# Performance work log

Measured on AMD Instinct MI355X. Metric: run time of the kernel, lower is better.

## Reference

```python
import jax, jax.numpy as jnp
import numpy as np

# Module config (matches init_kwargs)
G, K, S = 64, 3, 2          # base patch size, num scales, scale factor
B, H, W, C = 64, 512, 512, 3
HG, HL = 128, 128
D_IN = K * G * G * C


def setup_inputs() -> dict:
    key = jax.random.key(0)
    kx, kl, k1, k2 = jax.random.split(key, 4)
    x = jax.random.normal(kx, (B, H, W, C), dtype=jnp.float32)
    # glimpse locations in [-1, 1)
    l = jax.random.uniform(kl, (B, 2), minval=-1.0, maxval=1.0, dtype=jnp.float32)
    # fc1: phi (D_IN -> HG); fc2: l (2 -> HL). PyTorch-Linear-like scale.
    W1 = jax.random.normal(k1, (D_IN, HG), dtype=jnp.float32) / np.sqrt(D_IN)
    b1 = jnp.zeros((HG,), dtype=jnp.float32)
    W2 = jax.random.normal(k2, (2, HL), dtype=jnp.float32) / np.sqrt(2.0)
    b2 = jnp.zeros((HL,), dtype=jnp.float32)
    return {"x": x, "l": l, "W1": W1, "b1": b1, "W2": W2, "b2": b2}


def _extract_glimpse(x, l):
    """Retina: k multi-scale patches centered at l, resized to (G,G).
    Returns (B, K, G, G, C)."""
    sizes = [G * S**i for i in range(K)]              # 64, 128, 256
    pad = sizes[-1] // 2 + 1                          # pad once for largest scale
    xp = jnp.pad(x, ((0, 0), (pad, pad), (pad, pad), (0, 0)))
    # denormalize: [-1,1] -> [0,H], truncated to int (torch .long())
    coords = (0.5 * (l + 1.0) * H).astype(jnp.int32)  # (B,2): col0=x, col1=y
    patches = []
    for size in sizes:
        fy = coords[:, 1] - size // 2 + pad
        fx = coords[:, 0] - size // 2 + pad

        def slice_one(img, y0, x0, size=size):
            return jax.lax.dynamic_slice(img, (y0, x0, 0), (size, size, C))

        p = jax.vmap(slice_one)(xp, fy, fx)           # (B, size, size, C)
        f = size // G
        if f > 1:  # downsample by integer factor via average pooling
            p = p.reshape(B, G, f, G, f, C).mean(axis=(2, 4))
        patches.append(p)
    return jnp.stack(patches, axis=1)                 # (B, K, G, G, C)


def reference(x, l, W1, b1, W2, b2):
    phi = _extract_glimpse(x, l).reshape(x.shape[0], -1)   # (B, K*G*G*C)
    phi_out = jax.nn.relu(phi @ W1 + b1)                   # (B, HG)
    l_out = jax.nn.relu(l @ W2 + b2)                       # (B, HL)
    return jax.nn.relu(jnp.concatenate([phi_out, l_out], axis=1))
```

## Files before the change

kernel.cpp:

```cpp
#include <hip/hip_runtime.h>
#include <hip/hip_bf16.h>

#define G_     64
#define NK     3
#define NB     64
#define IH     512
#define IW     512
#define NC     3
#define HG_    128
#define HL_    128
#define D_IN_    (NK * G_ * G_ * NC)
#define D_SCALE  (G_ * G_ * NC)
#define KCH      128
#define NCHUNK   (D_IN_ / KCH)
#define BSPLIT   4
#define NBLK     (NCHUNK * BSPLIT)

__global__ void zero_acc(float* __restrict__ acc) {
    int i = blockIdx.x * 256 + threadIdx.x;
    if (i < NB * HG_) acc[i] = 0.0f;
}

template <int F>
__device__ __forceinline__ void scale_body(
    const float* __restrict__ x, const float* __restrict__ l,
    const float* __restrict__ W1, float* __restrict__ acc,
    int roff, int d0, int b0,
    float (&phi_s)[16][KCH], int* cx_s, int* cy_s)
{
    const int tid = threadIdx.x;
    if (tid < 16) {
        float lx = l[(b0 + tid) * 2 + 0];
        float ly = l[(b0 + tid) * 2 + 1];
        cx_s[tid] = (int)((0.5f * (lx + 1.0f)) * 512.0f);
        cy_s[tid] = (int)((0.5f * (ly + 1.0f)) * 512.0f);
    }
    __syncthreads();

    const int dd   = tid & (KCH - 1);
    const int jb0  = (tid >> 7) * 8;
    const int r    = roff + dd;
    const int gy   = r / (G_ * NC);
    const int rem  = r - gy * (G_ * NC);
    const int gx   = rem / NC;
    const int c    = rem - gx * NC;
    constexpr float inv = 1.0f / (float)(F * F);
    constexpr int JU = (F == 4) ? 2 : 8;

#pragma unroll 1
    for (int jo = 0; jo < 8; jo += JU) {
        float sums[JU];
#pragma unroll
        for (int ji = 0; ji < JU; ++ji) {
            const int jb = jb0 + jo + ji;
            const int b  = b0 + jb;
            const int by = cy_s[jb] - 32 * F + gy * F;
            const int bx = cx_s[jb] - 32 * F + gx * F;
            const float* bimg = x + (size_t)b * (IH * IW * NC) + c;
            float s = 0.0f;
#pragma unroll
            for (int dy = 0; dy < F; ++dy) {
                const int y = by + dy;
                const bool yok = (unsigned)y < (unsigned)IH;
#pragma unroll
                for (int dx = 0; dx < F; ++dx) {
                    const int xx = bx + dx;
                    const bool ok = yok && ((unsigned)xx < (unsigned)IW);
                    s += ok ? bimg[(size_t)y * (IW * NC) + xx * NC] : 0.0f;
                }
            }
            sums[ji] = s;
        }
#pragma unroll
        for (int ji = 0; ji < JU; ++ji)
            phi_s[jb0 + jo + ji][dd] = sums[ji] * inv;
    }
    __syncthreads();

    const int h0 = (tid & 31) * 4;
    const int bl = (tid >> 5) * 2;
    float a0[4] = {0, 0, 0, 0}, a1[4] = {0, 0, 0, 0};
    const float* wp = W1 + (size_t)d0 * HG_ + h0;
    const float4* prow0 = (const float4*)phi_s[bl];
    const float4* prow1 = (const float4*)phi_s[bl + 1];

#pragma unroll 2
    for (int t = 0; t < KCH / 4; ++t) {
        float4 p0v = prow0[t];
        float4 p1v = prow1[t];
#pragma unroll
        for (int u = 0; u < 4; ++u) {
            float4 wv = *(const float4*)(wp + (size_t)(4 * t + u) * HG_);
            float p0 = (&p0v.x)[u];
            float p1 = (&p1v.x)[u];
            a0[0] = fmaf(p0, wv.x, a0[0]);
            a0[1] = fmaf(p0, wv.y, a0[1]);
            a0[2] = fmaf(p0, wv.z, a0[2]);
            a0[3] = fmaf(p0, wv.w, a0[3]);
            a1[0] = fmaf(p1, wv.x, a1[0]);
            a1[1] = fmaf(p1, wv.y, a1[1]);
            a1[2] = fmaf(p1, wv.z, a1[2]);
            a1[3] = fmaf(p1, wv.w, a1[3]);
        }
    }
#pragma unroll
    for (int jj = 0; jj < 4; ++jj) {
        atomicAdd(&acc[(b0 + bl) * HG_ + h0 + jj], a0[jj]);
        atomicAdd(&acc[(b0 + bl + 1) * HG_ + h0 + jj], a1[jj]);
    }
}

__global__ __launch_bounds__(256) void fused(
    const float* __restrict__ x, const float* __restrict__ l,
    const float* __restrict__ W1, float* __restrict__ acc)
{
    __shared__ float phi_s[16][KCH];
    __shared__ int cx_s[16], cy_s[16];

    const int chunkGlobal = blockIdx.x >> 2;
    const int b0 = (blockIdx.x & 3) * 16;
    const int d0 = chunkGlobal * KCH;
    const int chunkLocal = chunkGlobal % 96;
    const int roff = chunkLocal * KCH;

    if (chunkGlobal < 96) {
        scale_body<1>(x, l, W1, acc, roff, d0, b0, phi_s, cx_s, cy_s);
    } else if (chunkGlobal < 192) {
        scale_body<2>(x, l, W1, acc, roff, d0, b0, phi_s, cx_s, cy_s);
    } else {
        scale_body<4>(x, l, W1, acc, roff, d0, b0, phi_s, cx_s, cy_s);
    }
}

__global__ void epilogue(
    const float* __restrict__ acc,
    const float* __restrict__ l,
    const float* __restrict__ b1,
    const float* __restrict__ W2,
    const float* __restrict__ b2,
    float* __restrict__ out)
{
    int idx = blockIdx.x * 256 + threadIdx.x;
    if (idx >= NB * (HG_ + HL_)) return;
    int b = idx >> 8;
    int h = idx & 255;
    float v;
    if (h < HG_) {
        v = acc[b * HG_ + h] + b1[h];
    } else {
        int hh = h - HG_;
        float l0 = l[b * 2 + 0];
        float l1 = l[b * 2 + 1];
        v = fmaf(l1, W2[HL_ + hh], fmaf(l0, W2[hh], b2[hh]));
    }
    out[idx] = fmaxf(v, 0.0f);
}

extern "C" void kernel_launch(void* const* d_in, const int* in_sizes, int n_in,
                              void* d_out, int out_size, void* d_ws, size_t ws_size,
                              hipStream_t stream) {
    const float* x  = (const float*)d_in[0];
    const float* l  = (const float*)d_in[1];
    const float* W1 = (const float*)d_in[2];
    const float* b1 = (const float*)d_in[3];
    const float* W2 = (const float*)d_in[4];
    const float* b2 = (const float*)d_in[5];
    float* out = (float*)d_out;
    float* acc = (float*)d_ws;

    zero_acc<<<(NB * HG_ + 255) / 256, 256, 0, stream>>>(acc);
    fused<<<NBLK, 256, 0, stream>>>(x, l, W1, acc);
    epilogue<<<(NB * (HG_ + HL_) + 255) / 256, 256, 0, stream>>>(acc, l, b1, W2, b2, out);
}
```

Baseline: 293.7 us.

## Replace atomic accumulation with per-chunk partials and a deterministic reduce epilogue

Each block now writes its partial products to a dedicated slice of a partial-sum buffer (288 chunks × 64×128) with float4 stores, instead of issuing float atomicAdds into a shared accumulator. The separate zero kernel is dropped, and the epilogue becomes one kernel that sums the 288 partials per batch row, split across two thread halves, before adding bias and applying ReLU. This removes atomic contention and one launch. In exchange it needs about 9.4 MB of workspace and a reduction pass that reads all of it.

```diff
diff --git a/kernel.cpp b/kernel.cpp
--- a/kernel.cpp
+++ b/kernel.cpp
@@ -15,17 +15,13 @@
 #define NCHUNK   (D_IN_ / KCH)
 #define BSPLIT   4
 #define NBLK     (NCHUNK * BSPLIT)
-
-__global__ void zero_acc(float* __restrict__ acc) {
-    int i = blockIdx.x * 256 + threadIdx.x;
-    if (i < NB * HG_) acc[i] = 0.0f;
-}
+#define PSTRIDE  (NB * HG_)
 
 template <int F>
 __device__ __forceinline__ void scale_body(
     const float* __restrict__ x, const float* __restrict__ l,
-    const float* __restrict__ W1, float* __restrict__ acc,
-    int roff, int d0, int b0,
+    const float* __restrict__ W1, float* __restrict__ P,
+    int roff, int d0, int b0, int chunkGlobal,
     float (&phi_s)[16][KCH], int* cx_s, int* cy_s)
 {
     const int tid = threadIdx.x;
@@ -103,16 +99,14 @@
             a1[3] = fmaf(p1, wv.w, a1[3]);
         }
     }
-#pragma unroll
-    for (int jj = 0; jj < 4; ++jj) {
-        atomicAdd(&acc[(b0 + bl) * HG_ + h0 + jj], a0[jj]);
-        atomicAdd(&acc[(b0 + bl + 1) * HG_ + h0 + jj], a1[jj]);
-    }
+    float* pb = P + (size_t)chunkGlobal * PSTRIDE + (b0 + bl) * HG_ + h0;
+    *(float4*)pb            = make_float4(a0[0], a0[1], a0[2], a0[3]);
+    *(float4*)(pb + HG_)    = make_float4(a1[0], a1[1], a1[2], a1[3]);
 }
 
 __global__ __launch_bounds__(256) void fused(
     const float* __restrict__ x, const float* __restrict__ l,
-    const float* __restrict__ W1, float* __restrict__ acc)
+    const float* __restrict__ W1, float* __restrict__ P)
 {
     __shared__ float phi_s[16][KCH];
     __shared__ int cx_s[16], cy_s[16];
@@ -124,36 +118,45 @@
     const int roff = chunkLocal * KCH;
 
     if (chunkGlobal < 96) {
-        scale_body<1>(x, l, W1, acc, roff, d0, b0, phi_s, cx_s, cy_s);
+        scale_body<1>(x, l, W1, P, roff, d0, b0, chunkGlobal, phi_s, cx_s, cy_s);
     } else if (chunkGlobal < 192) {
-        scale_body<2>(x, l, W1, acc, roff, d0, b0, phi_s, cx_s, cy_s);
+        scale_body<2>(x, l, W1, P, roff, d0, b0, chunkGlobal, phi_s, cx_s, cy_s);
     } else {
-        scale_body<4>(x, l, W1, acc, roff, d0, b0, phi_s, cx_s, cy_s);
+        scale_body<4>(x, l, W1, P, roff, d0, b0, chunkGlobal, phi_s, cx_s, cy_s);
     }
 }
 
-__global__ void epilogue(
-    const float* __restrict__ acc,
+__global__ __launch_bounds__(256) void reduce_epilogue(
+    const float* __restrict__ P,
     const float* __restrict__ l,
     const float* __restrict__ b1,
     const float* __restrict__ W2,
     const float* __restrict__ b2,
     float* __restrict__ out)
 {
-    int idx = blockIdx.x * 256 + threadIdx.x;
-    if (idx >= NB * (HG_ + HL_)) return;
-    int b = idx >> 8;
-    int h = idx & 255;
-    float v;
-    if (h < HG_) {
-        v = acc[b * HG_ + h] + b1[h];
+    __shared__ float red[HG_];
+    const int b = blockIdx.x;
+    const int t = threadIdx.x;
+    const int h = t & (HG_ - 1);
+    const int half = t >> 7;
+
+    float s = 0.0f;
+    const float* p = P + (size_t)(half * 144) * PSTRIDE + b * HG_ + h;
+#pragma unroll 8
+    for (int c = 0; c < 144; ++c)
+        s += p[(size_t)c * PSTRIDE];
+
+    if (half == 1) red[h] = s;
+    __syncthreads();
+
+    if (half == 0) {
+        out[b * (HG_ + HL_) + h] = fmaxf(s + red[h] + b1[h], 0.0f);
     } else {
-        int hh = h - HG_;
         float l0 = l[b * 2 + 0];
         float l1 = l[b * 2 + 1];
-        v = fmaf(l1, W2[HL_ + hh], fmaf(l0, W2[hh], b2[hh]));
+        float v = fmaf(l1, W2[HL_ + h], fmaf(l0, W2[h], b2[h]));
+        out[b * (HG_ + HL_) + HG_ + h] = fmaxf(v, 0.0f);
     }
-    out[idx] = fmaxf(v, 0.0f);
 }
 
 extern "C" void kernel_launch(void* const* d_in, const int* in_sizes, int n_in,
@@ -166,9 +169,8 @@
     const float* W2 = (const float*)d_in[4];
     const float* b2 = (const float*)d_in[5];
     float* out = (float*)d_out;
-    float* acc = (float*)d_ws;
+    float* P = (float*)d_ws;
 
-    zero_acc<<<(NB * HG_ + 255) / 256, 256, 0, stream>>>(acc);
-    fused<<<NBLK, 256, 0, stream>>>(x, l, W1, acc);
-    epilogue<<<(NB * (HG_ + HL_) + 255) / 256, 256, 0, stream>>>(acc, l, b1, W2, b2, out);
+    fused<<<NBLK, 256, 0, stream>>>(x, l, W1, P);
+    reduce_epilogue<<<NB, 256, 0, stream>>>(P, l, b1, W2, b2, out);
 }
```

After: 290.3 us. No clear change (-1.2%).
